# Kernel tuning notes

Hardware: AMD Instinct MI355X
Metric: run time of the kernel (lower is better)

The kernel has to match this reference:

```python
import jax, jax.numpy as jnp
import numpy as np
from jax import lax

MID = 64      # mid_size -> token seq len = MID*MID = 4096
DM = 64       # d_model = in_channels
DI = 128      # d_inner = expand * d_model
DS = 16       # d_state
DC = 4        # d_conv
DTR = 4       # dt_rank = ceil(DM/16)
EPS = 1e-5


def conv3x3(x, w):
    return lax.conv_general_dilated(x, w, (1, 1), ((1, 1), (1, 1)),
                                    dimension_numbers=('NCHW', 'OIHW', 'NCHW'))


def layernorm(x, w, b):
    mu = jnp.mean(x, -1, keepdims=True)
    var = jnp.mean((x - mu) ** 2, -1, keepdims=True)
    return (x - mu) * lax.rsqrt(var + EPS) * w + b


def bilinear(x, h, w):
    b, c = x.shape[:2]
    return jax.image.resize(x, (b, c, h, w), method='bilinear', antialias=False)


def mamba(tok, in_w, conv_w, conv_b, xproj_w, dt_w, dt_b, Alog, D, out_w):
    # tok: (b, L, DM)
    b, L, _ = tok.shape
    xz = tok @ in_w.T                                # (b, L, 2*DI)
    xc, z = jnp.split(xz, 2, axis=-1)
    # causal depthwise conv1d over sequence
    xcT = xc.transpose(0, 2, 1)                      # (b, DI, L)
    xconv = lax.conv_general_dilated(xcT, conv_w, (1,), ((DC - 1, 0),),
                                     dimension_numbers=('NCH', 'OIH', 'NCH'),
                                     feature_group_count=DI)
    xconv = xconv + conv_b[None, :, None]
    u = jax.nn.silu(xconv.transpose(0, 2, 1))        # (b, L, DI)
    x_dbl = u @ xproj_w.T                            # (b, L, DTR+2*DS)
    dt, B, C = jnp.split(x_dbl, [DTR, DTR + DS], axis=-1)
    dt = jax.nn.softplus(dt @ dt_w.T + dt_b)         # (b, L, DI)
    A = -jnp.exp(Alog)                               # (DI, DS)
    dA = jnp.exp(dt[..., None] * A)                  # (b, L, DI, DS)
    dBu = dt[..., None] * B[:, :, None, :] * u[..., None]

    def step(h, xs):
        a_t, bu_t = xs
        h = a_t * h + bu_t
        return h, h

    h0 = jnp.zeros((b, DI, DS), dt.dtype)
    _, hs = lax.scan(step, h0, (dA.transpose(1, 0, 2, 3), dBu.transpose(1, 0, 2, 3)))
    y = jnp.einsum('lbns,bls->bln', hs, C) + u * D   # (b, L, DI)
    y = y * jax.nn.silu(z)
    return y @ out_w.T                               # (b, L, DM)


def setup_inputs() -> dict:
    key = jax.random.key(0)
    ks = iter(jax.random.split(key, 32))
    s = 0.02
    d = {}
    d['x'] = jax.random.normal(next(ks), (4, 64, 128, 128), jnp.float32)
    for n, shp in [('cb_w1', (64, 64, 3, 3)), ('cb_w2', (64, 64, 3, 3)),
                   ('sm_w1', (64, 64, 3, 3)), ('sm_w2', (64, 64, 3, 3))]:
        d[n] = jax.random.normal(next(ks), shp, jnp.float32) * s
    d['ln1_w'] = jnp.ones((DM,), jnp.float32); d['ln1_b'] = jnp.zeros((DM,), jnp.float32)
    d['ln2_w'] = jnp.ones((DM,), jnp.float32); d['ln2_b'] = jnp.zeros((DM,), jnp.float32)
    for p in ['m1', 'm2']:
        d[p + '_in_w'] = jax.random.normal(next(ks), (2 * DI, DM), jnp.float32) * s
        d[p + '_conv_w'] = jax.random.normal(next(ks), (DI, 1, DC), jnp.float32) * s
        d[p + '_conv_b'] = jnp.zeros((DI,), jnp.float32)
        d[p + '_xproj_w'] = jax.random.normal(next(ks), (DTR + 2 * DS, DI), jnp.float32) * s
        d[p + '_dt_w'] = jax.random.normal(next(ks), (DI, DTR), jnp.float32) * s
        d[p + '_dt_b'] = jnp.full((DI,), -2.0, jnp.float32)
        d[p + '_Alog'] = jnp.broadcast_to(jnp.log(jnp.arange(1, DS + 1, dtype=jnp.float32)), (DI, DS)).copy()
        d[p + '_D'] = jnp.ones((DI,), jnp.float32)
        d[p + '_out_w'] = jax.random.normal(next(ks), (DM, DI), jnp.float32) * s
    return d


def reference(x, cb_w1, cb_w2, ln1_w, ln1_b, ln2_w, ln2_b,
              m1_in_w, m1_conv_w, m1_conv_b, m1_xproj_w, m1_dt_w, m1_dt_b, m1_Alog, m1_D, m1_out_w,
              m2_in_w, m2_conv_w, m2_conv_b, m2_xproj_w, m2_dt_w, m2_dt_b, m2_Alog, m2_D, m2_out_w,
              sm_w1, sm_w2):
    b, c, h, w = x.shape
    xr = conv3x3(jax.nn.relu(conv3x3(x, cb_w1)), cb_w2) + x
    x_small = xr if (h, w) == (MID, MID) else bilinear(xr, MID, MID)
    tokens = x_small.reshape(b, c, MID * MID).transpose(0, 2, 1)   # (b, L, c)
    main = mamba(layernorm(tokens, ln1_w, ln1_b),
                 m1_in_w, m1_conv_w, m1_conv_b, m1_xproj_w, m1_dt_w, m1_dt_b, m1_Alog, m1_D, m1_out_w)
    gate_feat = mamba(layernorm(tokens, ln2_w, ln2_b),
                      m2_in_w, m2_conv_w, m2_conv_b, m2_xproj_w, m2_dt_w, m2_dt_b, m2_Alog, m2_D, m2_out_w)
    gate = jax.nn.softmax(gate_feat, axis=1)                       # softmax over token dim
    tokens = tokens + gate * main
    feat = tokens.transpose(0, 2, 1).reshape(b, c, MID, MID)
    if (h, w) != (MID, MID):
        feat = bilinear(feat, h, w)
    return conv3x3(jax.nn.relu(conv3x3(feat, sm_w1)), sm_w2)
```

## Files before the change

### kernel.cpp

```cpp
#include <hip/hip_runtime.h>

typedef unsigned int u32;
typedef unsigned short u16;
typedef __attribute__((ext_vector_type(8))) short short8;
typedef __attribute__((ext_vector_type(4))) float f32x4;

__device__ __forceinline__ float sigmoidf_(float x){
  return 1.f / (1.f + __expf(-x));
}
__device__ __forceinline__ u16 f2bf(float f){
  union { float f; u32 i; } v; v.f = f;
  u32 r = v.i + 0x7fffu + ((v.i >> 16) & 1u);
  return (u16)(r >> 16);
}
__device__ __forceinline__ float bf2f(u32 u){
  union { float f; u32 i; } v; v.i = (u & 0xffffu) << 16; return v.f;
}
__device__ __forceinline__ float softplus_(float x){
  return fmaxf(x, 0.f) + __logf(1.f + __expf(-fabsf(x)));
}

__global__ void k_setup(const float* __restrict__ w0, u16* __restrict__ h0, u16* __restrict__ l0,
                        const float* __restrict__ w1, u16* __restrict__ h1, u16* __restrict__ l1,
                        const float* __restrict__ w2, u16* __restrict__ h2, u16* __restrict__ l2,
                        const float* __restrict__ w3, u16* __restrict__ h3, u16* __restrict__ l3,
                        const float* __restrict__ Wa, const float* __restrict__ lnwa, const float* __restrict__ lnba,
                        float* __restrict__ W2a, float* __restrict__ B2a,
                        const float* __restrict__ Wb, const float* __restrict__ lnwb, const float* __restrict__ lnbb,
                        float* __restrict__ W2b, float* __restrict__ B2b){
  int gidx = blockIdx.x * 256 + threadIdx.x;
  if (gidx < 147456){
    int set = gidx / 36864;
    int idx = gidx - set * 36864;
    const float* w; u16* WH; u16* WL;
    if (set == 0){ w = w0; WH = h0; WL = l0; }
    else if (set == 1){ w = w1; WH = h1; WL = l1; }
    else if (set == 2){ w = w2; WH = h2; WL = l2; }
    else { w = w3; WH = h3; WL = l3; }
    int j    = idx & 7;
    int lane = (idx >> 3) & 63;
    int nt   = (idx >> 9) & 3;
    int kc   = (idx >> 11) & 1;
    int t    = idx >> 12;
    int ic = kc * 32 + ((lane >> 4) & 3) * 8 + j;
    int oc = nt * 16 + (lane & 15);
    float v = w[(oc * 64 + ic) * 9 + t];
    u16 h = f2bf(v);
    u16 l = f2bf(v - bf2f(h));
    WH[idx] = h; WL[idx] = l;
  } else {
    int i = gidx - 147456;
    if (i >= 128) return;
    int m = i >> 6, j = i & 63;
    const float* W   = m ? Wb   : Wa;
    const float* lnw = m ? lnwb : lnwa;
    const float* lnb = m ? lnbb : lnba;
    float* W2 = m ? W2b : W2a;
    float* B2 = m ? B2b : B2a;
    float bias = 0.f;
#pragma unroll
    for (int k4 = 0; k4 < 16; k4++){
      float4 wv = *(const float4*)&W[j * 64 + k4 * 4];
      float4 gw = *(const float4*)&lnw[k4 * 4];
      float4 gb = *(const float4*)&lnb[k4 * 4];
      W2[j * 64 + k4 * 4 + 0] = wv.x * gw.x;
      W2[j * 64 + k4 * 4 + 1] = wv.y * gw.y;
      W2[j * 64 + k4 * 4 + 2] = wv.z * gw.z;
      W2[j * 64 + k4 * 4 + 3] = wv.w * gw.w;
      bias = fmaf(wv.x, gb.x, bias);
      bias = fmaf(wv.y, gb.y, bias);
      bias = fmaf(wv.z, gb.z, bias);
      bias = fmaf(wv.w, gb.w, bias);
    }
    B2[j] = bias;
  }
}

__global__ __launch_bounds__(256) void k_prep(const float* __restrict__ src,
                                              u16* __restrict__ PH, u16* __restrict__ PL,
                                              u16* __restrict__ BPH, u16* __restrict__ BPL){
  __shared__ float ld[64 * 129];
  int yp = blockIdx.x;
  int b  = blockIdx.y;
  int ys = yp - 1;
  int tid = threadIdx.x;
  if (yp == 0 || yp == 129){
    for (int i = tid; i < 130 * 64; i += 256){
      int x = i >> 6, c = i & 63;
      size_t o = (((size_t)b * 130 + yp) * 130 + x) * 64 + c;
      BPH[o] = 0; BPL[o] = 0;
    }
  } else {
    for (int i = tid; i < 128; i += 256){
      int x = (i >= 64) ? 129 : 0, c = i & 63;
      size_t o = (((size_t)b * 130 + yp) * 130 + x) * 64 + c;
      BPH[o] = 0; BPL[o] = 0;
    }
  }
  if ((u32)ys < 128u){
    for (int i = tid; i < 8192; i += 256){
      int c = i >> 7, x = i & 127;
      ld[c * 129 + x] = src[((size_t)(b * 64 + c) * 128 + ys) * 128 + x];
    }
  }
  __syncthreads();
  for (int i = tid; i < 130 * 64; i += 256){
    int xp = i >> 6, c = i & 63;
    float v = 0.f;
    if ((u32)ys < 128u && (u32)(xp - 1) < 128u) v = ld[c * 129 + (xp - 1)];
    u16 h = f2bf(v);
    u16 l = f2bf(v - bf2f(h));
    size_t o = (((size_t)b * 130 + yp) * 130 + xp) * 64 + c;
    PH[o] = h; PL[o] = l;
  }
}

__global__ __launch_bounds__(256) void k_prepup(const float* __restrict__ FEAT,
                                                u16* __restrict__ PH, u16* __restrict__ PL,
                                                u16* __restrict__ BPH, u16* __restrict__ BPL){
  __shared__ float ld0[64 * 65], ld1[64 * 65];
  int yp = blockIdx.x;
  int b  = blockIdx.y;
  int ys = yp - 1;
  int tid = threadIdx.x;
  if (yp == 0 || yp == 129){
    for (int i = tid; i < 130 * 64; i += 256){
      int x = i >> 6, c = i & 63;
      size_t o = (((size_t)b * 130 + yp) * 130 + x) * 64 + c;
      BPH[o] = 0; BPL[o] = 0;
    }
  } else {
    for (int i = tid; i < 128; i += 256){
      int x = (i >= 64) ? 129 : 0, c = i & 63;
      size_t o = (((size_t)b * 130 + yp) * 130 + x) * 64 + c;
      BPH[o] = 0; BPL[o] = 0;
    }
  }
  float wy = 0.f;
  if ((u32)ys < 128u){
    float ay = 0.5f * ys - 0.25f;
    int fy = (int)floorf(ay); wy = ay - fy;
    int y0s = fy < 0 ? 0 : fy, y1s = fy + 1 > 63 ? 63 : fy + 1;
    for (int i = tid; i < 1024; i += 256){
      int c = i >> 4, x4 = (i & 15) * 4;
      float4 a0 = *(const float4*)&FEAT[((size_t)(b * 64 + c) * 64 + y0s) * 64 + x4];
      float4 a1 = *(const float4*)&FEAT[((size_t)(b * 64 + c) * 64 + y1s) * 64 + x4];
      ld0[c * 65 + x4 + 0] = a0.x; ld0[c * 65 + x4 + 1] = a0.y;
      ld0[c * 65 + x4 + 2] = a0.z; ld0[c * 65 + x4 + 3] = a0.w;
      ld1[c * 65 + x4 + 0] = a1.x; ld1[c * 65 + x4 + 1] = a1.y;
      ld1[c * 65 + x4 + 2] = a1.z; ld1[c * 65 + x4 + 3] = a1.w;
    }
  }
  __syncthreads();
  for (int i = tid; i < 130 * 64; i += 256){
    int xp = i >> 6, c = i & 63;
    float v = 0.f;
    int xs = xp - 1;
    if ((u32)ys < 128u && (u32)xs < 128u){
      float ax = 0.5f * xs - 0.25f;
      int fx = (int)floorf(ax); float wx = ax - fx;
      int x0s = fx < 0 ? 0 : fx, x1s = fx + 1 > 63 ? 63 : fx + 1;
      float v0 = (1.f - wx) * ld0[c * 65 + x0s] + wx * ld0[c * 65 + x1s];
      float v1 = (1.f - wx) * ld1[c * 65 + x0s] + wx * ld1[c * 65 + x1s];
      v = (1.f - wy) * v0 + wy * v1;
    }
    u16 h = f2bf(v);
    u16 l = f2bf(v - bf2f(h));
    size_t o = (((size_t)b * 130 + yp) * 130 + xp) * 64 + c;
    PH[o] = h; PL[o] = l;
  }
}

__global__ __launch_bounds__(256) void k_convm(
    const u16* __restrict__ PH, const u16* __restrict__ PL,
    const u16* __restrict__ WH, const u16* __restrict__ WL,
    const float* __restrict__ resid,
    u16* __restrict__ OBH, u16* __restrict__ OBL,
    float* __restrict__ OUTF, float* __restrict__ T, float* __restrict__ NT,
    int mode)
{
  __shared__ __align__(16) u32 smem[17344];
  u16* Ah_s = (u16*)smem;
  u16* Al_s = Ah_s + 10368;
  int tid = threadIdx.x;
  int lane = tid & 63, w = tid >> 6;
  int quad = lane >> 4, lcol = lane & 15;
  int b = blockIdx.z, y0 = blockIdx.y * 16, x0 = blockIdx.x * 16;

  f32x4 acc[4][4];
#pragma unroll
  for (int mt = 0; mt < 4; mt++)
#pragma unroll
    for (int nt = 0; nt < 4; nt++)
      acc[mt][nt] = (f32x4){0.f, 0.f, 0.f, 0.f};

  for (int kc = 0; kc < 2; kc++){
    __syncthreads();
    for (int i = tid; i < 1296; i += 256){
      int q = i & 3;
      int rc = i >> 2;
      int r = rc / 18, c = rc - r * 18;
      size_t so = (((size_t)b * 130 + y0 + r) * 130 + (x0 + c)) * 64 + kc * 32 + q * 8;
      int de = rc * 32 + q * 8;
      *(uint4*)(Ah_s + de) = *(const uint4*)(PH + so);
      *(uint4*)(Al_s + de) = *(const uint4*)(PL + so);
    }
    __syncthreads();
#pragma unroll
    for (int t = 0; t < 9; t++){
      int dy = t / 3, dx = t - dy * 3;
      short8 bh[4], bl[4];
#pragma unroll
      for (int nt = 0; nt < 4; nt++){
        int o = ((t * 2 + kc) * 4 + nt) * 512 + lane * 8;
        bh[nt] = *(const short8*)(WH + o);
        bl[nt] = *(const short8*)(WL + o);
      }
      short8 ah[4], al[4];
#pragma unroll
      for (int mt = 0; mt < 4; mt++){
        int e = ((w * 4 + mt + dy) * 18 + (lcol + dx)) * 32 + quad * 8;
        ah[mt] = *(const short8*)(Ah_s + e);
        al[mt] = *(const short8*)(Al_s + e);
      }
#pragma unroll
      for (int mt = 0; mt < 4; mt++)
#pragma unroll
        for (int nt = 0; nt < 4; nt++){
          acc[mt][nt] = __builtin_amdgcn_mfma_f32_16x16x32_bf16(ah[mt], bh[nt], acc[mt][nt], 0, 0, 0);
          acc[mt][nt] = __builtin_amdgcn_mfma_f32_16x16x32_bf16(ah[mt], bl[nt], acc[mt][nt], 0, 0, 0);
          acc[mt][nt] = __builtin_amdgcn_mfma_f32_16x16x32_bf16(al[mt], bh[nt], acc[mt][nt], 0, 0, 0);
        }
    }
  }

  __syncthreads();
  if (mode == 0){
    u32* epi = smem;
#pragma unroll
    for (int mt = 0; mt < 4; mt++){
      int row = w * 4 + mt;
#pragma unroll
      for (int nt = 0; nt < 4; nt++){
#pragma unroll
        for (int reg = 0; reg < 4; reg++){
          float v = fmaxf(acc[mt][nt][reg], 0.f);
          u32 h = f2bf(v);
          u32 l = f2bf(v - bf2f(h));
          int ccol = quad * 4 + reg;
          int oc = nt * 16 + lcol;
          epi[(row * 16 + ccol) * 66 + oc] = h | (l << 16);
        }
      }
    }
    __syncthreads();
    for (int i = tid; i < 16384; i += 256){
      int px = i >> 6, oc = i & 63;
      int row = px >> 4, ccol = px & 15;
      u32 pk = epi[px * 66 + oc];
      size_t o = (((size_t)b * 130 + y0 + row + 1) * 130 + (x0 + ccol + 1)) * 64 + oc;
      OBH[o] = (u16)pk;
      OBL[o] = (u16)(pk >> 16);
    }
  } else {
    float* epi = (float*)smem;
#pragma unroll
    for (int mt = 0; mt < 4; mt++){
      int row = w * 4 + mt;
#pragma unroll
      for (int nt = 0; nt < 4; nt++){
#pragma unroll
        for (int reg = 0; reg < 4; reg++){
          int px = row * 16 + quad * 4 + reg;
          int oc = nt * 16 + lcol;
          epi[oc * 259 + px] = acc[mt][nt][reg];
        }
      }
    }
    __syncthreads();
    if (mode == 1){
      for (int i = tid; i < 16384; i += 256){
        int oc = i >> 8, px = i & 255;
        int row = px >> 4, c = px & 15;
        size_t o = (((size_t)b * 64 + oc) * 128 + y0 + row) * 128 + x0 + c;
        float v = epi[oc * 259 + px];
        if (resid) v += resid[o];
        OUTF[o] = v;
      }
    } else {
      for (int i = tid; i < 16384; i += 256){
        int oc = i >> 8, px = i & 255;
        int row = px >> 4, c = px & 15;
        size_t o = (((size_t)b * 64 + oc) * 128 + y0 + row) * 128 + x0 + c;
        epi[oc * 259 + px] += resid[o];
      }
      __syncthreads();
      float* redS  = (float*)smem + 16576;
      float* redQ  = redS + 320;
      float* stats = redQ + 320;
      int token = tid & 63, cg2 = tid >> 6;
      int tr = token >> 3, tc = token & 7;
      float av[16]; float s = 0.f, q = 0.f;
      int p0 = (2 * tr) * 16 + 2 * tc;
#pragma unroll
      for (int j = 0; j < 16; j++){
        int c = cg2 * 16 + ((j + tr) & 15);
        const float* ep = epi + c * 259;
        float v = 0.25f * (ep[p0] + ep[p0 + 1] + ep[p0 + 16] + ep[p0 + 17]);
        av[j] = v; s += v; q = fmaf(v, v, q);
      }
      redS[token * 5 + cg2] = s;
      redQ[token * 5 + cg2] = q;
      __syncthreads();
      if (tid < 64){
        float S = 0.f, Q = 0.f;
        for (int g = 0; g < 4; g++){ S += redS[tid * 5 + g]; Q += redQ[tid * 5 + g]; }
        float mu = S * (1.f / 64.f);
        float var = Q * (1.f / 64.f) - mu * mu;
        stats[tid * 2] = mu;
        stats[tid * 2 + 1] = rsqrtf(var + 1e-5f);
      }
      __syncthreads();
      float mu = stats[token * 2], inv = stats[token * 2 + 1];
      int l = (blockIdx.y * 8 + tr) * 64 + blockIdx.x * 8 + tc;
      size_t to = ((size_t)b * 4096 + l) * 64;
#pragma unroll
      for (int j = 0; j < 16; j++){
        int c = cg2 * 16 + ((j + tr) & 15);
        T[to + c] = av[j];
        NT[to + c] = (av[j] - mu) * inv;
      }
    }
  }
}

__global__ __launch_bounds__(256) void k_inprojdw(
    const float* __restrict__ NT,
    const float* __restrict__ W2a, const float* __restrict__ B2a,
    float* __restrict__ Ua, float* __restrict__ Za,
    const float* __restrict__ cwa, const float* __restrict__ cba,
    const float* __restrict__ W2b, const float* __restrict__ B2b,
    float* __restrict__ Ub, float* __restrict__ Zb,
    const float* __restrict__ cwb, const float* __restrict__ cbb)
{
  __shared__ float wL[64 * 68];
  __shared__ float xcs[67 * 68];
  int mz = blockIdx.z;
  const float* W2 = mz ? W2b : W2a;
  const float* B2 = mz ? B2b : B2a;
  float* U = mz ? Ub : Ua;
  float* Z  = mz ? Zb : Za;
  const float* cw = mz ? cwb : cwa;
  const float* cb = mz ? cbb : cba;
  int tid = threadIdx.x;
  int t0 = blockIdx.x * 64;
  int j0 = blockIdx.y * 64;
  for (int i = tid; i < 4096; i += 256){
    int jl = i >> 6, k = i & 63;
    wL[jl * 68 + k] = W2[(size_t)(j0 + jl) * 64 + k];
  }
  __syncthreads();
  int tq = tid >> 4, cg = tid & 15;
  const float* ntp = NT + (size_t)(t0 + tq * 4) * 64;
  float acc[4][4];
#pragma unroll
  for (int c = 0; c < 4; c++){
    float bias = B2[j0 + cg + c * 16];
#pragma unroll
    for (int t = 0; t < 4; t++) acc[t][c] = bias;
  }
#pragma unroll 4
  for (int k4 = 0; k4 < 16; k4++){
    float4 lv[4];
#pragma unroll
    for (int t = 0; t < 4; t++)
      lv[t] = *(const float4*)(ntp + t * 64 + k4 * 4);
    float4 wv[4];
#pragma unroll
    for (int c = 0; c < 4; c++)
      wv[c] = *(const float4*)&wL[(cg + c * 16) * 68 + k4 * 4];
#pragma unroll
    for (int t = 0; t < 4; t++)
#pragma unroll
      for (int c = 0; c < 4; c++){
        acc[t][c] = fmaf(lv[t].x, wv[c].x, acc[t][c]);
        acc[t][c] = fmaf(lv[t].y, wv[c].y, acc[t][c]);
        acc[t][c] = fmaf(lv[t].z, wv[c].z, acc[t][c]);
        acc[t][c] = fmaf(lv[t].w, wv[c].w, acc[t][c]);
      }
  }
  if (j0 < 128){
    int isStart = ((t0 & 4095) == 0);
    if (tid < 192){
      int e = tid >> 6, col = tid & 63;
      float v = 0.f;
      if (!isStart){
        const float* np = NT + (size_t)(t0 - 3 + e) * 64;
        float a2 = B2[j0 + col];
#pragma unroll 4
        for (int k = 0; k < 64; k += 4){
          float4 nv = *(const float4*)(np + k);
          float4 wv = *(const float4*)&wL[col * 68 + k];
          a2 = fmaf(nv.x, wv.x, fmaf(nv.y, wv.y, fmaf(nv.z, wv.z, fmaf(nv.w, wv.w, a2))));
        }
        v = a2;
      }
      xcs[e * 68 + col] = v;
    }
#pragma unroll
    for (int t = 0; t < 4; t++)
#pragma unroll
      for (int c = 0; c < 4; c++)
        xcs[(3 + tq * 4 + t) * 68 + cg + c * 16] = acc[t][c];
    __syncthreads();
#pragma unroll
    for (int c = 0; c < 4; c++){
      int lc = cg + c * 16;
      int ch = j0 + lc;
      float4 wv = *(const float4*)(cw + ch * 4);
      float bias = cb[ch];
#pragma unroll
      for (int t = 0; t < 4; t++){
        int row = 3 + tq * 4 + t;
        float a = bias;
        a = fmaf(wv.w, xcs[row * 68 + lc], a);
        a = fmaf(wv.z, xcs[(row - 1) * 68 + lc], a);
        a = fmaf(wv.y, xcs[(row - 2) * 68 + lc], a);
        a = fmaf(wv.x, xcs[(row - 3) * 68 + lc], a);
        size_t tg = t0 + tq * 4 + t;
        U[tg * 128 + ch] = a * sigmoidf_(a);
      }
    }
  } else {
#pragma unroll
    for (int t = 0; t < 4; t++){
      size_t tg = t0 + tq * 4 + t;
#pragma unroll
      for (int c = 0; c < 4; c++)
        Z[tg * 128 + (j0 - 128) + cg + c * 16] = acc[t][c];
    }
  }
}

__global__ __launch_bounds__(256) void k_xprojdt(
    const float* __restrict__ U0, const float* __restrict__ XW0, float* __restrict__ DBL0,
    const float* __restrict__ U1, const float* __restrict__ XW1, float* __restrict__ DBL1)
{
  __shared__ float xw[36 * 132];
  int bid = blockIdx.x;
  int m = bid >> 7, blk = bid & 127;
  const float* Up   = m ? U1   : U0;
  const float* XWp  = m ? XW1  : XW0;
  float* DBLp = m ? DBL1 : DBL0;
  int tid = threadIdx.x;
  for (int i = tid; i < 4608; i += 256)
    xw[(i >> 7) * 132 + (i & 127)] = XWp[i];
  __syncthreads();
  int slot = tid >> 2, jq = tid & 3;
  size_t tgA = (size_t)blk * 128 + slot;
  size_t tgB = tgA + 64;
  const float4* upA = (const float4*)(Up + tgA * 128);
  const float4* upB = (const float4*)(Up + tgB * 128);
  float accA[9], accB[9];
#pragma unroll
  for (int jj = 0; jj < 9; jj++){ accA[jj] = 0.f; accB[jj] = 0.f; }
  for (int k4 = 0; k4 < 32; k4++){
    float4 uA = upA[k4];
    float4 uB = upB[k4];
#pragma unroll
    for (int jj = 0; jj < 9; jj++){
      float4 w = *(const float4*)&xw[(jq * 9 + jj) * 132 + k4 * 4];
      accA[jj] = fmaf(w.x, uA.x, fmaf(w.y, uA.y, fmaf(w.z, uA.z, fmaf(w.w, uA.w, accA[jj]))));
      accB[jj] = fmaf(w.x, uB.x, fmaf(w.y, uB.y, fmaf(w.z, uB.z, fmaf(w.w, uB.w, accB[jj]))));
    }
  }
#pragma unroll
  for (int jj = 0; jj < 9; jj++){
    DBLp[tgA * 36 + jq * 9 + jj] = accA[jj];
    DBLp[tgB * 36 + jq * 9 + jj] = accB[jj];
  }
}

__global__ __launch_bounds__(256) void k_scanA(
    const float* __restrict__ DBL0, const float* __restrict__ U0, const float* __restrict__ AL0,
    const float* __restrict__ DTW0, const float* __restrict__ DTB0,
    const float* __restrict__ DBL1, const float* __restrict__ U1, const float* __restrict__ AL1,
    const float* __restrict__ DTW1, const float* __restrict__ DTB1,
    float* __restrict__ HF, float* __restrict__ AP)
{
  __shared__ float su[32 * 65], sB[16 * 36], sdtr[128];
  int bid = blockIdx.x;
  int cg = bid & 1;
  int c  = (bid >> 1) & 127;
  int b  = (bid >> 8) & 3;
  int m  = bid >> 10;
  const float* DBLp = m ? DBL1 : DBL0;
  const float* Up   = m ? U1   : U0;
  const float* ALp  = m ? AL1  : AL0;
  const float* DTWp = m ? DTW1 : DTW0;
  const float* DTBp = m ? DTB1 : DTB0;
  int tid = threadIdx.x;
  int lane = tid & 63, w = tid >> 6;
  int lcol = lane & 15, q = lane >> 4;
  int chL = w * 16 + lcol;
  int n = cg * 64 + chL;
  size_t base = (size_t)b * 4096 + c * 32;
  for (int i = tid; i < 2048; i += 256){
    int ch = i & 63, l = i >> 6;
    su[l * 65 + ch] = Up[(base + l) * 128 + cg * 64 + ch];
  }
  for (int i = tid; i < 512; i += 256){
    int s = i & 15, l = i >> 4;
    sB[s * 36 + l] = DBLp[(base + l) * 36 + 4 + s];
  }
  if (tid < 128){
    int l = tid >> 2, jj = tid & 3;
    sdtr[tid] = DBLp[(base + l) * 36 + jj];
  }
  const float LOG2E = 1.4426950408889634f;
  float A1[4];
  bool fastp = true;
#pragma unroll
  for (int j = 0; j < 4; j++){
    A1[j] = -__expf(ALp[n * 16 + q * 4 + j]) * LOG2E;
    float expe = -(float)(q * 4 + j + 1) * LOG2E;
    fastp = fastp && (fabsf(A1[j] - expe) <= 1e-3f);
  }
  float4 wdt = *(const float4*)(DTWp + n * 4);
  float bdt = DTBp[n];
  __syncthreads();
  float h[4] = {0.f, 0.f, 0.f, 0.f};
  float ap[4] = {1.f, 1.f, 1.f, 1.f};
#pragma unroll
  for (int l4 = 0; l4 < 8; l4++){
    int lq = l4 * 4 + q;
    float4 dq = *(const float4*)&sdtr[lq * 4];
    float xq = bdt;
    xq = fmaf(wdt.x, dq.x, xq); xq = fmaf(wdt.y, dq.y, xq);
    xq = fmaf(wdt.z, dq.z, xq); xq = fmaf(wdt.w, dq.w, xq);
    float dtq = softplus_(xq);
    float rq = __expf(-dtq);
    float dts[4], rs[4];
    dts[0] = __shfl(dtq, lcol);       rs[0] = __shfl(rq, lcol);
    dts[1] = __shfl(dtq, lcol + 16);  rs[1] = __shfl(rq, lcol + 16);
    dts[2] = __shfl(dtq, lcol + 32);  rs[2] = __shfl(rq, lcol + 32);
    dts[3] = __shfl(dtq, lcol + 48);  rs[3] = __shfl(rq, lcol + 48);
    float4 Bv[4];
#pragma unroll
    for (int j = 0; j < 4; j++) Bv[j] = *(const float4*)&sB[(q * 4 + j) * 36 + l4 * 4];
    if (fastp){
#pragma unroll
      for (int jj = 0; jj < 4; jj++){
        int l = l4 * 4 + jj;
        float dt = dts[jj], r = rs[jj];
        float u  = su[l * 65 + chL];
        float dtu = dt * u;
        float r2 = r * r, r4 = r2 * r2;
        float r8 = r4 * r4;
        float p0 = (q == 0) ? r : (q == 1) ? r4 * r : (q == 2) ? r8 * r : (r8 * r4) * r;
        float a0 = p0, a1 = a0 * r, a2 = a1 * r, a3 = a2 * r;
        h[0] = fmaf(a0, h[0], dtu * (&Bv[0].x)[jj]); ap[0] *= a0;
        h[1] = fmaf(a1, h[1], dtu * (&Bv[1].x)[jj]); ap[1] *= a1;
        h[2] = fmaf(a2, h[2], dtu * (&Bv[2].x)[jj]); ap[2] *= a2;
        h[3] = fmaf(a3, h[3], dtu * (&Bv[3].x)[jj]); ap[3] *= a3;
      }
    } else {
#pragma unroll
      for (int jj = 0; jj < 4; jj++){
        int l = l4 * 4 + jj;
        float dt = dts[jj];
        float u  = su[l * 65 + chL];
        float dtu = dt * u;
#pragma unroll
        for (int j = 0; j < 4; j++){
          float a = exp2f(dt * A1[j]);
          h[j] = fmaf(a, h[j], dtu * (&Bv[j].x)[jj]);
          ap[j] *= a;
        }
      }
    }
  }
  size_t o = ((size_t)((m * 4 + b) * 128 + c)) * 2048 + n * 16 + q * 4;
  *(float4*)&HF[o] = make_float4(h[0], h[1], h[2], h[3]);
  *(float4*)&AP[o] = make_float4(ap[0], ap[1], ap[2], ap[3]);
}

__global__ __launch_bounds__(64) void k_scanB(
    const float* __restrict__ HF, const float* __restrict__ AP, float* __restrict__ HIN)
{
  int r = blockIdx.x * 64 + threadIdx.x;
  int q = r >> 11;
  int p = r & 2047;
  size_t base = (size_t)q * 128 * 2048 + p;
  float h = 0.f;
  for (int c8 = 0; c8 < 16; c8++){
    float a[8], f[8];
#pragma unroll
    for (int j = 0; j < 8; j++){
      size_t o = base + (size_t)(c8 * 8 + j) * 2048;
      a[j] = AP[o]; f[j] = HF[o];
    }
#pragma unroll
    for (int j = 0; j < 8; j++){
      size_t o = base + (size_t)(c8 * 8 + j) * 2048;
      HIN[o] = h;
      h = fmaf(a[j], h, f[j]);
    }
  }
}

__global__ __launch_bounds__(256) void k_scanC(
    const float* __restrict__ DBL0, const float* __restrict__ U0, const float* __restrict__ AL0,
    const float* __restrict__ DTW0, const float* __restrict__ DTB0,
    const float* __restrict__ D0, float* __restrict__ Y0,
    const float* __restrict__ DBL1, const float* __restrict__ U1, const float* __restrict__ AL1,
    const float* __restrict__ DTW1, const float* __restrict__ DTB1,
    const float* __restrict__ D1, float* __restrict__ Y1,
    const float* __restrict__ HIN)
{
  __shared__ float su[32 * 65], sB[16 * 36], sC[16 * 36], sdtr[128];
  int bid = blockIdx.x;
  int cg = bid & 1;
  int c  = (bid >> 1) & 127;
  int b  = (bid >> 8) & 3;
  int m  = bid >> 10;
  const float* DBLp = m ? DBL1 : DBL0;
  const float* Up   = m ? U1   : U0;
  const float* ALp  = m ? AL1  : AL0;
  const float* DTWp = m ? DTW1 : DTW0;
  const float* DTBp = m ? DTB1 : DTB0;
  const float* Dp   = m ? D1   : D0;
  float*       Yp   = m ? Y1   : Y0;
  int tid = threadIdx.x;
  int lane = tid & 63, w = tid >> 6;
  int lcol = lane & 15, q = lane >> 4;
  int chL = w * 16 + lcol;
  int n = cg * 64 + chL;
  size_t base = (size_t)b * 4096 + c * 32;
  for (int i = tid; i < 2048; i += 256){
    int ch = i & 63, l = i >> 6;
    su[l * 65 + ch] = Up[(base + l) * 128 + cg * 64 + ch];
  }
  for (int i = tid; i < 512; i += 256){
    int s = i & 15, l = i >> 4;
    size_t ob = (base + l) * 36;
    sB[s * 36 + l] = DBLp[ob + 4 + s];
    sC[s * 36 + l] = DBLp[ob + 20 + s];
  }
  if (tid < 128){
    int l = tid >> 2, jj = tid & 3;
    sdtr[tid] = DBLp[(base + l) * 36 + jj];
  }
  const float LOG2E = 1.4426950408889634f;
  float A1[4];
  bool fastp = true;
#pragma unroll
  for (int j = 0; j < 4; j++){
    A1[j] = -__expf(ALp[n * 16 + q * 4 + j]) * LOG2E;
    float expe = -(float)(q * 4 + j + 1) * LOG2E;
    fastp = fastp && (fabsf(A1[j] - expe) <= 1e-3f);
  }
  float4 wdt = *(const float4*)(DTWp + n * 4);
  float bdt = DTBp[n];
  float Dn = Dp[n];
  float4 hv = *(const float4*)&HIN[((size_t)((m * 4 + b) * 128 + c)) * 2048 + n * 16 + q * 4];
  float h[4] = {hv.x, hv.y, hv.z, hv.w};
  __syncthreads();
#pragma unroll
  for (int l4 = 0; l4 < 8; l4++){
    int lq = l4 * 4 + q;
    float4 dq = *(const float4*)&sdtr[lq * 4];
    float xq = bdt;
    xq = fmaf(wdt.x, dq.x, xq); xq = fmaf(wdt.y, dq.y, xq);
    xq = fmaf(wdt.z, dq.z, xq); xq = fmaf(wdt.w, dq.w, xq);
    float dtq = softplus_(xq);
    float rq = __expf(-dtq);
    float dts[4], rs[4];
    dts[0] = __shfl(dtq, lcol);       rs[0] = __shfl(rq, lcol);
    dts[1] = __shfl(dtq, lcol + 16);  rs[1] = __shfl(rq, lcol + 16);
    dts[2] = __shfl(dtq, lcol + 32);  rs[2] = __shfl(rq, lcol + 32);
    dts[3] = __shfl(dtq, lcol + 48);  rs[3] = __shfl(rq, lcol + 48);
    float4 Bv[4], Cv[4];
#pragma unroll
    for (int j = 0; j < 4; j++){
      Bv[j] = *(const float4*)&sB[(q * 4 + j) * 36 + l4 * 4];
      Cv[j] = *(const float4*)&sC[(q * 4 + j) * 36 + l4 * 4];
    }
    if (fastp){
#pragma unroll
      for (int jj = 0; jj < 4; jj++){
        int l = l4 * 4 + jj;
        float dt = dts[jj], r = rs[jj];
        float u  = su[l * 65 + chL];
        float dtu = dt * u;
        float r2 = r * r, r4 = r2 * r2;
        float r8 = r4 * r4;
        float p0 = (q == 0) ? r : (q == 1) ? r4 * r : (q == 2) ? r8 * r : (r8 * r4) * r;
        float a0 = p0, a1 = a0 * r, a2 = a1 * r, a3 = a2 * r;
        float p = 0.f;
        h[0] = fmaf(a0, h[0], dtu * (&Bv[0].x)[jj]); p = fmaf(h[0], (&Cv[0].x)[jj], p);
        h[1] = fmaf(a1, h[1], dtu * (&Bv[1].x)[jj]); p = fmaf(h[1], (&Cv[1].x)[jj], p);
        h[2] = fmaf(a2, h[2], dtu * (&Bv[2].x)[jj]); p = fmaf(h[2], (&Cv[2].x)[jj], p);
        h[3] = fmaf(a3, h[3], dtu * (&Bv[3].x)[jj]); p = fmaf(h[3], (&Cv[3].x)[jj], p);
        p += __shfl_xor(p, 16);
        p += __shfl_xor(p, 32);
        if (q == 0)
          Yp[(base + l) * 128 + n] = fmaf(u, Dn, p);
      }
    } else {
#pragma unroll
      for (int jj = 0; jj < 4; jj++){
        int l = l4 * 4 + jj;
        float dt = dts[jj];
        float u  = su[l * 65 + chL];
        float dtu = dt * u;
        float p = 0.f;
#pragma unroll
        for (int j = 0; j < 4; j++){
          float a = exp2f(dt * A1[j]);
          h[j] = fmaf(a, h[j], dtu * (&Bv[j].x)[jj]);
          p = fmaf(h[j], (&Cv[j].x)[jj], p);
        }
        p += __shfl_xor(p, 16);
        p += __shfl_xor(p, 32);
        if (q == 0)
          Yp[(base + l) * 128 + n] = fmaf(u, Dn, p);
      }
    }
  }
}

__global__ __launch_bounds__(256) void k_outproj(
    const float* __restrict__ Y0, const float* __restrict__ Zg0,
    const float* __restrict__ W0, float* __restrict__ OUT0,
    const float* __restrict__ Y1, const float* __restrict__ Zg1,
    const float* __restrict__ W1, float* __restrict__ OUT1)
{
  __shared__ float yl[16 * 128];
  __shared__ float wT[128 * 65];
  int m = blockIdx.y;
  const float* Y  = m ? Y1  : Y0;
  const float* Zg = m ? Zg1 : Zg0;
  const float* W  = m ? W1  : W0;
  float* OUT = m ? OUT1 : OUT0;
  int tid = threadIdx.x;
  size_t t0 = (size_t)blockIdx.x * 16;
  for (int i = tid; i < 2048; i += 256){
    float z = Zg[t0 * 128 + i];
    yl[i] = Y[t0 * 128 + i] * (z * sigmoidf_(z));
  }
  for (int i = tid; i < 8192; i += 256){
    int k = i & 127, j = i >> 7;
    wT[k * 65 + j] = W[j * 128 + k];
  }
  __syncthreads();
  int j = tid & 63;
  int tg = tid >> 6;
  float acc[4] = {0.f, 0.f, 0.f, 0.f};
  for (int k = 0; k < 128; k += 4){
    float w0 = wT[k * 65 + j], w1 = wT[(k+1) * 65 + j];
    float w2 = wT[(k+2) * 65 + j], w3 = wT[(k+3) * 65 + j];
#pragma unroll
    for (int t = 0; t < 4; t++){
      float4 yv = *(const float4*)&yl[(tg * 4 + t) * 128 + k];
      acc[t] = fmaf(w0, yv.x, fmaf(w1, yv.y, fmaf(w2, yv.z, fmaf(w3, yv.w, acc[t]))));
    }
  }
#pragma unroll
  for (int t = 0; t < 4; t++)
    OUT[(t0 + tg * 4 + t) * 64 + j] = acc[t];
}

__global__ void k_smA(const float* __restrict__ G, float* __restrict__ P){
  int bid = blockIdx.x;
  int b = bid >> 6, lc = bid & 63;
  int tid = threadIdx.x;
  int j = tid & 63, part = tid >> 6;
  size_t base = (size_t)b * 4096 + lc * 64;
  float mx = -3.4e38f;
  for (int i = 0; i < 16; i++){
    int l = part + i * 4;
    mx = fmaxf(mx, G[(base + l) * 64 + j]);
  }
  float sm = 0.f;
  for (int i = 0; i < 16; i++){
    int l = part + i * 4;
    sm += __expf(G[(base + l) * 64 + j] - mx);
  }
  __shared__ float sM[256], sS[256];
  sM[tid] = mx; sS[tid] = sm;
  __syncthreads();
  if (tid < 64){
    float M = sM[tid], S = sS[tid];
    for (int p = 1; p < 4; p++){
      float m2 = sM[p * 64 + tid], s2 = sS[p * 64 + tid];
      float Mn = fmaxf(M, m2);
      S = S * __expf(M - Mn) + s2 * __expf(m2 - Mn);
      M = Mn;
    }
    P[(bid * 64 + tid) * 2] = M;
    P[(bid * 64 + tid) * 2 + 1] = S;
  }
}

__global__ void k_combine(const float* __restrict__ T, const float* __restrict__ MAIN,
                          const float* __restrict__ G, const float* __restrict__ P,
                          float* __restrict__ FEAT){
  int bid = blockIdx.x;
  int b = bid >> 6, row = bid & 63;
  int tid = threadIdx.x;
  __shared__ float tile[64 * 65];
  __shared__ float sM[256], sS[256], Mv[64], iSv[64];
  {
    int j2 = tid & 63, part = tid >> 6;
    float M = -3.4e38f, S = 0.f;
    for (int i = 0; i < 16; i++){
      int lc = part + i * 4;
      int idx = ((b * 64 + lc) * 64 + j2) * 2;
      float m2 = P[idx], s2 = P[idx + 1];
      float Mn = fmaxf(M, m2);
      S = S * __expf(M - Mn) + s2 * __expf(m2 - Mn);
      M = Mn;
    }
    sM[tid] = M; sS[tid] = S;
  }
  __syncthreads();
  if (tid < 64){
    float M = sM[tid], S = sS[tid];
    for (int p = 1; p < 4; p++){
      float m2 = sM[p * 64 + tid], s2 = sS[p * 64 + tid];
      float Mn = fmaxf(M, m2);
      S = S * __expf(M - Mn) + s2 * __expf(m2 - Mn);
      M = Mn;
    }
    Mv[tid] = M; iSv[tid] = 1.f / S;
  }
  __syncthreads();
  int j = tid & 63, ls = tid >> 6;
  float M = Mv[j], invS = iSv[j];
  size_t lbase = (size_t)b * 4096 + row * 64;
  for (int i = 0; i < 16; i++){
    int col = ls + i * 4;
    size_t off = (lbase + col) * 64 + j;
    float g = __expf(G[off] - M) * invS;
    tile[col * 65 + j] = T[off] + g * MAIN[off];
  }
  __syncthreads();
  int colw = tid & 63, jr = tid >> 6;
  for (int jj = jr; jj < 64; jj += 4)
    FEAT[(((size_t)b * 64 + jj) * 64 + row) * 64 + colw] = tile[colw * 65 + jj];
}

extern "C" void kernel_launch(void* const* d_in, const int* in_sizes, int n_in,
                              void* d_out, int out_size, void* d_ws, size_t ws_size,
                              hipStream_t stream) {
  const size_t P1A = 0, P1B = 4326400;
  const size_t MB0 = 0, MB1 = 10027008;
  const size_t O_LN = 0, O_XC = 1048576, O_Z = 3145728, O_U = 5242880,
               O_DBL = 9437184;
  const size_t TOK = 20054016, OUT0 = 21102592, OUT1 = 22151168;
  const size_t FEAT = 23208448;
  const size_t P3A = 4194304, P3B = 8520704;
  const size_t WSET = 19000000;
  const size_t PADN = 2163200;
  const size_t SMP = 0;
  const size_t W2_0 = 21102592, B2_0 = 21118976, W2_1 = 21119232, B2_1 = 21135616;
  const size_t TOTAL = 24257024;
  if (ws_size < TOTAL * 4) return;

  float* ws = (float*)d_ws;
  const float* X   = (const float*)d_in[0];
  const float* CB1 = (const float*)d_in[1];
  const float* CB2 = (const float*)d_in[2];
  const float* SW1 = (const float*)d_in[3];
  const float* SW2 = (const float*)d_in[4];
  const float* LNW[2] = { (const float*)d_in[5], (const float*)d_in[7] };
  const float* LNB[2] = { (const float*)d_in[6], (const float*)d_in[8] };
  const float *INW[2], *CW[2], *CBb[2], *XPW[2], *DTW[2], *DTB[2], *AL[2], *DD[2], *OW[2];
  for (int m = 0; m < 2; m++){
    int p = 9 + m * 9;
    INW[m] = (const float*)d_in[p + 0];
    CW[m]  = (const float*)d_in[p + 1];
    CBb[m] = (const float*)d_in[p + 2];
    XPW[m] = (const float*)d_in[p + 3];
    DTW[m] = (const float*)d_in[p + 4];
    DTB[m] = (const float*)d_in[p + 5];
    AL[m]  = (const float*)d_in[p + 6];
    DD[m]  = (const float*)d_in[p + 7];
    OW[m]  = (const float*)d_in[p + 8];
  }

  u16* wset[8];
  for (int k = 0; k < 8; k++) wset[k] = (u16*)(ws + WSET + (size_t)k * 18432);

  u16* p1ah = (u16*)(ws + P1A); u16* p1al = p1ah + PADN * 2;
  u16* p1bh = (u16*)(ws + P1B); u16* p1bl = p1bh + PADN * 2;
  u16* p3ah = (u16*)(ws + P3A); u16* p3al = p3ah + PADN * 2;
  u16* p3bh = (u16*)(ws + P3B); u16* p3bl = p3bh + PADN * 2;

  k_setup<<<577, 256, 0, stream>>>(CB1, wset[0], wset[1], CB2, wset[2], wset[3],
                                   SW1, wset[4], wset[5], SW2, wset[6], wset[7],
                                   INW[0], LNW[0], LNB[0], ws + W2_0, ws + B2_0,
                                   INW[1], LNW[1], LNB[1], ws + W2_1, ws + B2_1);

  k_prep<<<dim3(130, 4), 256, 0, stream>>>(X, p1ah, p1al, p1bh, p1bl);
  k_convm<<<dim3(8, 8, 4), 256, 0, stream>>>(p1ah, p1al, wset[0], wset[1], nullptr,
                                             p1bh, p1bl, nullptr, nullptr, nullptr, 0);
  k_convm<<<dim3(8, 8, 4), 256, 0, stream>>>(p1bh, p1bl, wset[2], wset[3], X,
                                             nullptr, nullptr, nullptr,
                                             ws + TOK, ws + MB0 + O_LN, 2);

  k_inprojdw<<<dim3(256, 4, 2), 256, 0, stream>>>(
      ws + MB0 + O_LN,
      ws + W2_0, ws + B2_0, ws + MB0 + O_U, ws + MB0 + O_Z, CW[0], CBb[0],
      ws + W2_1, ws + B2_1, ws + MB1 + O_U, ws + MB1 + O_Z, CW[1], CBb[1]);
  k_xprojdt<<<256, 256, 0, stream>>>(
      ws + MB0 + O_U, XPW[0], ws + MB0 + O_DBL,
      ws + MB1 + O_U, XPW[1], ws + MB1 + O_DBL);

  float* HF  = ws + MB0 + O_XC;
  float* AP  = ws + MB1 + O_XC;
  float* HIN = ws + OUT1;

  k_scanA<<<2048, 256, 0, stream>>>(
      ws + MB0 + O_DBL, ws + MB0 + O_U, AL[0], DTW[0], DTB[0],
      ws + MB1 + O_DBL, ws + MB1 + O_U, AL[1], DTW[1], DTB[1],
      HF, AP);
  k_scanB<<<256, 64, 0, stream>>>(HF, AP, HIN);
  k_scanC<<<2048, 256, 0, stream>>>(
      ws + MB0 + O_DBL, ws + MB0 + O_U, AL[0], DTW[0], DTB[0], DD[0], ws + MB0 + O_XC,
      ws + MB1 + O_DBL, ws + MB1 + O_U, AL[1], DTW[1], DTB[1], DD[1], ws + MB1 + O_XC,
      HIN);

  k_outproj<<<dim3(1024, 2), 256, 0, stream>>>(
      ws + MB0 + O_XC, ws + MB0 + O_Z, OW[0], ws + OUT0,
      ws + MB1 + O_XC, ws + MB1 + O_Z, OW[1], ws + OUT1);

  k_smA<<<256, 256, 0, stream>>>(ws + OUT1, ws + SMP);
  k_combine<<<256, 256, 0, stream>>>(ws + TOK, ws + OUT0, ws + OUT1, ws + SMP, ws + FEAT);

  k_prepup<<<dim3(130, 4), 256, 0, stream>>>(ws + FEAT, p3ah, p3al, p3bh, p3bl);
  k_convm<<<dim3(8, 8, 4), 256, 0, stream>>>(p3ah, p3al, wset[4], wset[5], nullptr,
                                             p3bh, p3bl, nullptr, nullptr, nullptr, 0);
  k_convm<<<dim3(8, 8, 4), 256, 0, stream>>>(p3bh, p3bl, wset[6], wset[7], nullptr,
                                             nullptr, nullptr, (float*)d_out,
                                             nullptr, nullptr, 1);
}
```

Baseline: 368.7 us.

## Fuse prep into setup, parallelize chunk scan, fold softmax stats into outproj

Merges the input padding/bf16-split kernel into the weight setup kernel, removing one launch. Rewrites the inter-chunk carry scan so 8 threads cooperate per state with a shuffle-based parallel prefix, replacing a 128-step serial loop over 256 small blocks. Computes the per-block softmax max/sum partials inside the out-projection epilogue instead of a separate kernel re-reading the gate output, and the combine kernel then reduces more, finer partials. The out-projection gains shared memory and an extra barrier on one branch.

```diff
diff --git a/kernel.cpp b/kernel.cpp
--- a/kernel.cpp
+++ b/kernel.cpp
@@ -20,98 +20,102 @@
   return fmaxf(x, 0.f) + __logf(1.f + __expf(-fabsf(x)));
 }
 
-__global__ void k_setup(const float* __restrict__ w0, u16* __restrict__ h0, u16* __restrict__ l0,
-                        const float* __restrict__ w1, u16* __restrict__ h1, u16* __restrict__ l1,
-                        const float* __restrict__ w2, u16* __restrict__ h2, u16* __restrict__ l2,
-                        const float* __restrict__ w3, u16* __restrict__ h3, u16* __restrict__ l3,
-                        const float* __restrict__ Wa, const float* __restrict__ lnwa, const float* __restrict__ lnba,
-                        float* __restrict__ W2a, float* __restrict__ B2a,
-                        const float* __restrict__ Wb, const float* __restrict__ lnwb, const float* __restrict__ lnbb,
-                        float* __restrict__ W2b, float* __restrict__ B2b){
-  int gidx = blockIdx.x * 256 + threadIdx.x;
-  if (gidx < 147456){
-    int set = gidx / 36864;
-    int idx = gidx - set * 36864;
-    const float* w; u16* WH; u16* WL;
-    if (set == 0){ w = w0; WH = h0; WL = l0; }
-    else if (set == 1){ w = w1; WH = h1; WL = l1; }
-    else if (set == 2){ w = w2; WH = h2; WL = l2; }
-    else { w = w3; WH = h3; WL = l3; }
-    int j    = idx & 7;
-    int lane = (idx >> 3) & 63;
-    int nt   = (idx >> 9) & 3;
-    int kc   = (idx >> 11) & 1;
-    int t    = idx >> 12;
-    int ic = kc * 32 + ((lane >> 4) & 3) * 8 + j;
-    int oc = nt * 16 + (lane & 15);
-    float v = w[(oc * 64 + ic) * 9 + t];
-    u16 h = f2bf(v);
-    u16 l = f2bf(v - bf2f(h));
-    WH[idx] = h; WL[idx] = l;
+__global__ __launch_bounds__(256) void k_setup(
+    const float* __restrict__ w0, u16* __restrict__ h0, u16* __restrict__ l0,
+    const float* __restrict__ w1, u16* __restrict__ h1, u16* __restrict__ l1,
+    const float* __restrict__ w2, u16* __restrict__ h2, u16* __restrict__ l2,
+    const float* __restrict__ w3, u16* __restrict__ h3, u16* __restrict__ l3,
+    const float* __restrict__ Wa, const float* __restrict__ lnwa, const float* __restrict__ lnba,
+    float* __restrict__ W2a, float* __restrict__ B2a,
+    const float* __restrict__ Wb, const float* __restrict__ lnwb, const float* __restrict__ lnbb,
+    float* __restrict__ W2b, float* __restrict__ B2b,
+    const float* __restrict__ src, u16* __restrict__ PH, u16* __restrict__ PL,
+    u16* __restrict__ BPH, u16* __restrict__ BPL)
+{
+  __shared__ float ld[64 * 129];
+  int bx = blockIdx.x;
+  int tid = threadIdx.x;
+  if (bx < 577){
+    int gidx = bx * 256 + tid;
+    if (gidx < 147456){
+      int set = gidx / 36864;
+      int idx = gidx - set * 36864;
+      const float* w; u16* WH; u16* WL;
+      if (set == 0){ w = w0; WH = h0; WL = l0; }
+      else if (set == 1){ w = w1; WH = h1; WL = l1; }
+      else if (set == 2){ w = w2; WH = h2; WL = l2; }
+      else { w = w3; WH = h3; WL = l3; }
+      int j    = idx & 7;
+      int lane = (idx >> 3) & 63;
+      int nt   = (idx >> 9) & 3;
+      int kc   = (idx >> 11) & 1;
+      int t    = idx >> 12;
+      int ic = kc * 32 + ((lane >> 4) & 3) * 8 + j;
+      int oc = nt * 16 + (lane & 15);
+      float v = w[(oc * 64 + ic) * 9 + t];
+      u16 h = f2bf(v);
+      u16 l = f2bf(v - bf2f(h));
+      WH[idx] = h; WL[idx] = l;
+    } else {
+      int i = gidx - 147456;
+      if (i >= 128) return;
+      int m = i >> 6, j = i & 63;
+      const float* W   = m ? Wb   : Wa;
+      const float* lnw = m ? lnwb : lnwa;
+      const float* lnb = m ? lnbb : lnba;
+      float* W2 = m ? W2b : W2a;
+      float* B2 = m ? B2b : B2a;
+      float bias = 0.f;
+#pragma unroll
+      for (int k4 = 0; k4 < 16; k4++){
+        float4 wv = *(const float4*)&W[j * 64 + k4 * 4];
+        float4 gw = *(const float4*)&lnw[k4 * 4];
+        float4 gb = *(const float4*)&lnb[k4 * 4];
+        W2[j * 64 + k4 * 4 + 0] = wv.x * gw.x;
+        W2[j * 64 + k4 * 4 + 1] = wv.y * gw.y;
+        W2[j * 64 + k4 * 4 + 2] = wv.z * gw.z;
+        W2[j * 64 + k4 * 4 + 3] = wv.w * gw.w;
+        bias = fmaf(wv.x, gb.x, bias);
+        bias = fmaf(wv.y, gb.y, bias);
+        bias = fmaf(wv.z, gb.z, bias);
+        bias = fmaf(wv.w, gb.w, bias);
+      }
+      B2[j] = bias;
+    }
   } else {
-    int i = gidx - 147456;
-    if (i >= 128) return;
-    int m = i >> 6, j = i & 63;
-    const float* W   = m ? Wb   : Wa;
-    const float* lnw = m ? lnwb : lnwa;
-    const float* lnb = m ? lnbb : lnba;
-    float* W2 = m ? W2b : W2a;
-    float* B2 = m ? B2b : B2a;
-    float bias = 0.f;
-#pragma unroll
-    for (int k4 = 0; k4 < 16; k4++){
-      float4 wv = *(const float4*)&W[j * 64 + k4 * 4];
-      float4 gw = *(const float4*)&lnw[k4 * 4];
-      float4 gb = *(const float4*)&lnb[k4 * 4];
-      W2[j * 64 + k4 * 4 + 0] = wv.x * gw.x;
-      W2[j * 64 + k4 * 4 + 1] = wv.y * gw.y;
-      W2[j * 64 + k4 * 4 + 2] = wv.z * gw.z;
-      W2[j * 64 + k4 * 4 + 3] = wv.w * gw.w;
-      bias = fmaf(wv.x, gb.x, bias);
-      bias = fmaf(wv.y, gb.y, bias);
-      bias = fmaf(wv.z, gb.z, bias);
-      bias = fmaf(wv.w, gb.w, bias);
-    }
-    B2[j] = bias;
-  }
-}
-
-__global__ __launch_bounds__(256) void k_prep(const float* __restrict__ src,
-                                              u16* __restrict__ PH, u16* __restrict__ PL,
-                                              u16* __restrict__ BPH, u16* __restrict__ BPL){
-  __shared__ float ld[64 * 129];
-  int yp = blockIdx.x;
-  int b  = blockIdx.y;
-  int ys = yp - 1;
-  int tid = threadIdx.x;
-  if (yp == 0 || yp == 129){
+    int bid2 = bx - 577;
+    int yp = bid2 % 130;
+    int b  = bid2 / 130;
+    int ys = yp - 1;
+    if (yp == 0 || yp == 129){
+      for (int i = tid; i < 130 * 64; i += 256){
+        int x = i >> 6, c = i & 63;
+        size_t o = (((size_t)b * 130 + yp) * 130 + x) * 64 + c;
+        BPH[o] = 0; BPL[o] = 0;
+      }
+    } else {
+      for (int i = tid; i < 128; i += 256){
+        int x = (i >= 64) ? 129 : 0, c = i & 63;
+        size_t o = (((size_t)b * 130 + yp) * 130 + x) * 64 + c;
+        BPH[o] = 0; BPL[o] = 0;
+      }
+    }
+    if ((u32)ys < 128u){
+      for (int i = tid; i < 8192; i += 256){
+        int c = i >> 7, x = i & 127;
+        ld[c * 129 + x] = src[((size_t)(b * 64 + c) * 128 + ys) * 128 + x];
+      }
+    }
+    __syncthreads();
     for (int i = tid; i < 130 * 64; i += 256){
-      int x = i >> 6, c = i & 63;
-      size_t o = (((size_t)b * 130 + yp) * 130 + x) * 64 + c;
-      BPH[o] = 0; BPL[o] = 0;
-    }
-  } else {
-    for (int i = tid; i < 128; i += 256){
-      int x = (i >= 64) ? 129 : 0, c = i & 63;
-      size_t o = (((size_t)b * 130 + yp) * 130 + x) * 64 + c;
-      BPH[o] = 0; BPL[o] = 0;
-    }
-  }
-  if ((u32)ys < 128u){
-    for (int i = tid; i < 8192; i += 256){
-      int c = i >> 7, x = i & 127;
-      ld[c * 129 + x] = src[((size_t)(b * 64 + c) * 128 + ys) * 128 + x];
-    }
-  }
-  __syncthreads();
-  for (int i = tid; i < 130 * 64; i += 256){
-    int xp = i >> 6, c = i & 63;
-    float v = 0.f;
-    if ((u32)ys < 128u && (u32)(xp - 1) < 128u) v = ld[c * 129 + (xp - 1)];
-    u16 h = f2bf(v);
-    u16 l = f2bf(v - bf2f(h));
-    size_t o = (((size_t)b * 130 + yp) * 130 + xp) * 64 + c;
-    PH[o] = h; PL[o] = l;
+      int xp = i >> 6, c = i & 63;
+      float v = 0.f;
+      if ((u32)ys < 128u && (u32)(xp - 1) < 128u) v = ld[c * 129 + (xp - 1)];
+      u16 h = f2bf(v);
+      u16 l = f2bf(v - bf2f(h));
+      size_t o = (((size_t)b * 130 + yp) * 130 + xp) * 64 + c;
+      PH[o] = h; PL[o] = l;
+    }
   }
 }
 
@@ -585,27 +589,41 @@
   *(float4*)&AP[o] = make_float4(ap[0], ap[1], ap[2], ap[3]);
 }
 
-__global__ __launch_bounds__(64) void k_scanB(
+__global__ __launch_bounds__(256) void k_scanB(
     const float* __restrict__ HF, const float* __restrict__ AP, float* __restrict__ HIN)
 {
-  int r = blockIdx.x * 64 + threadIdx.x;
+  int gid = blockIdx.x * 256 + threadIdx.x;
+  int r = gid >> 3;
+  int seg = gid & 7;
   int q = r >> 11;
   int p = r & 2047;
-  size_t base = (size_t)q * 128 * 2048 + p;
-  float h = 0.f;
-  for (int c8 = 0; c8 < 16; c8++){
-    float a[8], f[8];
+  size_t base = (size_t)q * 128 * 2048 + p + (size_t)seg * 16 * 2048;
+  float a[16], f[16];
+#pragma unroll
+  for (int c8 = 0; c8 < 2; c8++){
 #pragma unroll
     for (int j = 0; j < 8; j++){
       size_t o = base + (size_t)(c8 * 8 + j) * 2048;
-      a[j] = AP[o]; f[j] = HF[o];
-    }
-#pragma unroll
-    for (int j = 0; j < 8; j++){
-      size_t o = base + (size_t)(c8 * 8 + j) * 2048;
-      HIN[o] = h;
-      h = fmaf(a[j], h, f[j]);
-    }
+      a[c8 * 8 + j] = AP[o];
+      f[c8 * 8 + j] = HF[o];
+    }
+  }
+  float A = 1.f, F = 0.f;
+#pragma unroll
+  for (int j = 0; j < 16; j++){ F = fmaf(a[j], F, f[j]); A *= a[j]; }
+#pragma unroll
+  for (int d = 1; d < 8; d <<= 1){
+    float Au = __shfl_up(A, d, 8);
+    float Fu = __shfl_up(F, d, 8);
+    if (seg >= d){ F = fmaf(A, Fu, F); A = A * Au; }
+  }
+  float hin = __shfl_up(F, 1, 8);
+  float h = (seg == 0) ? 0.f : hin;
+#pragma unroll
+  for (int j = 0; j < 16; j++){
+    size_t o = base + (size_t)j * 2048;
+    HIN[o] = h;
+    h = fmaf(a[j], h, f[j]);
   }
 }
 
@@ -734,10 +752,12 @@
     const float* __restrict__ Y0, const float* __restrict__ Zg0,
     const float* __restrict__ W0, float* __restrict__ OUT0,
     const float* __restrict__ Y1, const float* __restrict__ Zg1,
-    const float* __restrict__ W1, float* __restrict__ OUT1)
+    const float* __restrict__ W1, float* __restrict__ OUT1,
+    float* __restrict__ P)
 {
   __shared__ float yl[16 * 128];
   __shared__ float wT[128 * 65];
+  __shared__ float rM[256], rS[256];
   int m = blockIdx.y;
   const float* Y  = m ? Y1  : Y0;
   const float* Zg = m ? Zg1 : Zg0;
@@ -769,37 +789,22 @@
 #pragma unroll
   for (int t = 0; t < 4; t++)
     OUT[(t0 + tg * 4 + t) * 64 + j] = acc[t];
-}
-
-__global__ void k_smA(const float* __restrict__ G, float* __restrict__ P){
-  int bid = blockIdx.x;
-  int b = bid >> 6, lc = bid & 63;
-  int tid = threadIdx.x;
-  int j = tid & 63, part = tid >> 6;
-  size_t base = (size_t)b * 4096 + lc * 64;
-  float mx = -3.4e38f;
-  for (int i = 0; i < 16; i++){
-    int l = part + i * 4;
-    mx = fmaxf(mx, G[(base + l) * 64 + j]);
-  }
-  float sm = 0.f;
-  for (int i = 0; i < 16; i++){
-    int l = part + i * 4;
-    sm += __expf(G[(base + l) * 64 + j] - mx);
-  }
-  __shared__ float sM[256], sS[256];
-  sM[tid] = mx; sS[tid] = sm;
-  __syncthreads();
-  if (tid < 64){
-    float M = sM[tid], S = sS[tid];
-    for (int p = 1; p < 4; p++){
-      float m2 = sM[p * 64 + tid], s2 = sS[p * 64 + tid];
-      float Mn = fmaxf(M, m2);
-      S = S * __expf(M - Mn) + s2 * __expf(m2 - Mn);
-      M = Mn;
-    }
-    P[(bid * 64 + tid) * 2] = M;
-    P[(bid * 64 + tid) * 2 + 1] = S;
+  if (m == 1){
+    float mx = fmaxf(fmaxf(acc[0], acc[1]), fmaxf(acc[2], acc[3]));
+    float sm = __expf(acc[0] - mx) + __expf(acc[1] - mx) + __expf(acc[2] - mx) + __expf(acc[3] - mx);
+    rM[tid] = mx; rS[tid] = sm;
+    __syncthreads();
+    if (tid < 64){
+      float M = rM[tid], S = rS[tid];
+      for (int p2 = 1; p2 < 4; p2++){
+        float m2 = rM[p2 * 64 + tid], s2 = rS[p2 * 64 + tid];
+        float Mn = fmaxf(M, m2);
+        S = S * __expf(M - Mn) + s2 * __expf(m2 - Mn);
+        M = Mn;
+      }
+      P[((size_t)blockIdx.x * 64 + tid) * 2] = M;
+      P[((size_t)blockIdx.x * 64 + tid) * 2 + 1] = S;
+    }
   }
 }
 
@@ -814,9 +819,9 @@
   {
     int j2 = tid & 63, part = tid >> 6;
     float M = -3.4e38f, S = 0.f;
-    for (int i = 0; i < 16; i++){
-      int lc = part + i * 4;
-      int idx = ((b * 64 + lc) * 64 + j2) * 2;
+    for (int i = 0; i < 64; i++){
+      int pb = part + i * 4;
+      int idx = ((b * 256 + pb) * 64 + j2) * 2;
       float m2 = P[idx], s2 = P[idx + 1];
       float Mn = fmaxf(M, m2);
       S = S * __expf(M - Mn) + s2 * __expf(m2 - Mn);
@@ -898,12 +903,12 @@
   u16* p3ah = (u16*)(ws + P3A); u16* p3al = p3ah + PADN * 2;
   u16* p3bh = (u16*)(ws + P3B); u16* p3bl = p3bh + PADN * 2;
 
-  k_setup<<<577, 256, 0, stream>>>(CB1, wset[0], wset[1], CB2, wset[2], wset[3],
-                                   SW1, wset[4], wset[5], SW2, wset[6], wset[7],
-                                   INW[0], LNW[0], LNB[0], ws + W2_0, ws + B2_0,
-                                   INW[1], LNW[1], LNB[1], ws + W2_1, ws + B2_1);
-
-  k_prep<<<dim3(130, 4), 256, 0, stream>>>(X, p1ah, p1al, p1bh, p1bl);
+  k_setup<<<1097, 256, 0, stream>>>(CB1, wset[0], wset[1], CB2, wset[2], wset[3],
+                                    SW1, wset[4], wset[5], SW2, wset[6], wset[7],
+                                    INW[0], LNW[0], LNB[0], ws + W2_0, ws + B2_0,
+                                    INW[1], LNW[1], LNB[1], ws + W2_1, ws + B2_1,
+                                    X, p1ah, p1al, p1bh, p1bl);
+
   k_convm<<<dim3(8, 8, 4), 256, 0, stream>>>(p1ah, p1al, wset[0], wset[1], nullptr,
                                              p1bh, p1bl, nullptr, nullptr, nullptr, 0);
   k_convm<<<dim3(8, 8, 4), 256, 0, stream>>>(p1bh, p1bl, wset[2], wset[3], X,
@@ -926,7 +931,7 @@
       ws + MB0 + O_DBL, ws + MB0 + O_U, AL[0], DTW[0], DTB[0],
       ws + MB1 + O_DBL, ws + MB1 + O_U, AL[1], DTW[1], DTB[1],
       HF, AP);
-  k_scanB<<<256, 64, 0, stream>>>(HF, AP, HIN);
+  k_scanB<<<512, 256, 0, stream>>>(HF, AP, HIN);
   k_scanC<<<2048, 256, 0, stream>>>(
       ws + MB0 + O_DBL, ws + MB0 + O_U, AL[0], DTW[0], DTB[0], DD[0], ws + MB0 + O_XC,
       ws + MB1 + O_DBL, ws + MB1 + O_U, AL[1], DTW[1], DTB[1], DD[1], ws + MB1 + O_XC,
@@ -934,9 +939,9 @@
 
   k_outproj<<<dim3(1024, 2), 256, 0, stream>>>(
       ws + MB0 + O_XC, ws + MB0 + O_Z, OW[0], ws + OUT0,
-      ws + MB1 + O_XC, ws + MB1 + O_Z, OW[1], ws + OUT1);
-
-  k_smA<<<256, 256, 0, stream>>>(ws + OUT1, ws + SMP);
+      ws + MB1 + O_XC, ws + MB1 + O_Z, OW[1], ws + OUT1,
+      ws + SMP);
+
   k_combine<<<256, 256, 0, stream>>>(ws + TOK, ws + OUT0, ws + OUT1, ws + SMP, ws + FEAT);
 
   k_prepup<<<dim3(130, 4), 256, 0, stream>>>(ws + FEAT, p3ah, p3al, p3bh, p3bl);
```

Measured after the change: 366.2 us. About the same (-0.7%).
